# Performance work log

Hardware: AMD Instinct MI355X
Metric: run time of the kernel (lower is better)

Reference implementation:

```python
import jax, jax.numpy as jnp
import numpy as np

S, B, IN, HID, H, D, DFF, L, NC, EMB = 1024, 32, 3072, 256, 16, 16, 1024, 4, 1623, 10


def setup_inputs() -> dict:
    key = jax.random.key(0)
    ks = jax.random.split(key, 12)
    w = lambda k, shp: 0.02 * jax.random.normal(k, shp, dtype=jnp.float32)
    return {
        "x": jax.random.normal(ks[0], (S, B, IN), dtype=jnp.float32),
        "fb": jax.random.randint(ks[1], (S, B), 0, NC),
        "fc1_w": w(ks[2], (HID, IN)),
        "fc1_b": jnp.zeros((HID,), jnp.float32),
        "emb": w(ks[3], (NC, EMB)),
        "proj_w": w(ks[4], (HID, HID + EMB)),
        "proj_b": jnp.zeros((HID,), jnp.float32),
        "ln1_g": jnp.ones((L, HID), jnp.float32),
        "ln1_b": jnp.zeros((L, HID), jnp.float32),
        "slow_w": w(ks[5], (L, H * (3 * D + 1), HID)),
        "out_w": w(ks[6], (L, HID, H * D)),
        "ln2_g": jnp.ones((L, HID), jnp.float32),
        "ln2_b": jnp.zeros((L, HID), jnp.float32),
        "ff1_w": w(ks[7], (L, DFF, HID)),
        "ff1_b": jnp.zeros((L, DFF), jnp.float32),
        "ff2_w": w(ks[8], (L, HID, DFF)),
        "ff2_b": jnp.zeros((L, HID), jnp.float32),
        "outl_w": w(ks[9], (NC, HID)),
        "outl_b": jnp.zeros((NC,), jnp.float32),
    }


def _ln(x, g, b):
    m = jnp.mean(x, -1, keepdims=True)
    v = jnp.mean(jnp.square(x - m), -1, keepdims=True)
    return (x - m) * jax.lax.rsqrt(v + 1e-5) * g + b


def _delta_attn(x, g, b, sw, ow):
    # x: (S, B, HID); delta-rule fast-weight linear attention
    s, bsz, _ = x.shape
    qkvb = jnp.einsum('sbi,oi->sbo', _ln(x, g, b), sw).reshape(s, bsz, H, 3 * D + 1)
    q, k, v, beta = jnp.split(qkvb, [D, 2 * D, 3 * D], axis=-1)
    q = jax.nn.softmax(q, axis=-1)      # sum-normalized feature map
    k = jax.nn.softmax(k, axis=-1)
    beta = jax.nn.sigmoid(beta)         # (S,B,H,1)

    def step(W, inp):
        qt, kt, vt, bt = inp            # (B,H,D),(B,H,D),(B,H,D),(B,H,1)
        v_old = jnp.einsum('bhkv,bhk->bhv', W, kt)
        v_new = bt * vt + (1.0 - bt) * v_old
        W = W + jnp.einsum('bhk,bhv->bhkv', kt, v_new - v_old)
        return W, jnp.einsum('bhkv,bhk->bhv', W, qt)

    W0 = jnp.zeros((bsz, H, D, D), x.dtype)
    _, o = jax.lax.scan(step, W0, (q, k, v, beta))   # o: (S,B,H,D)
    return x + jnp.einsum('sbi,oi->sbo', o.reshape(s, bsz, H * D), ow)


def _ffn(x, g, b, w1, b1, w2, b2):
    h = jax.nn.relu(jnp.einsum('sbi,oi->sbo', _ln(x, g, b), w1) + b1)
    return x + jnp.einsum('sbi,oi->sbo', h, w2) + b2


def reference(x, fb, fc1_w, fc1_b, emb, proj_w, proj_b, ln1_g, ln1_b, slow_w,
              out_w, ln2_g, ln2_b, ff1_w, ff1_b, ff2_w, ff2_b, outl_w, outl_b):
    h = jnp.einsum('sbi,oi->sbo', x, fc1_w) + fc1_b
    h = jnp.concatenate([h, emb[fb]], axis=-1)
    h = jnp.einsum('sbi,oi->sbo', h, proj_w) + proj_b
    for l in range(L):
        h = _delta_attn(h, ln1_g[l], ln1_b[l], slow_w[l], out_w[l])
        h = _ffn(h, ln2_g[l], ln2_b[l], ff1_w[l], ff1_b[l], ff2_w[l], ff2_b[l])
    return jnp.einsum('sbi,oi->sbo', h, outl_w) + outl_b
```

## Files before the change

### kernel.cpp

```cpp
#include <hip/hip_runtime.h>
#include <hip/hip_bf16.h>

#define S_LEN  1024
#define B_SZ   32
#define IN_DIM 3072
#define HID    256
#define NHEAD  16
#define HDIM   16
#define DFF    1024
#define NLAYER 4
#define NCLS   1623
#define EMB_D  10
#define MROWS  (S_LEN * B_SZ)
#define QSTRIDE 52

using bf16   = __hip_bfloat16;
using short8 = __attribute__((ext_vector_type(8))) short;
using f32x4  = __attribute__((ext_vector_type(4))) float;

#define GLOAD16(g, l) __builtin_amdgcn_global_load_lds(                        \
    (const __attribute__((address_space(1))) void*)(g),                        \
    (__attribute__((address_space(3))) void*)(l), 16, 0, 0)

template<int FLAGS>
__global__ __launch_bounds__(256) void mgemm(
    const bf16* __restrict__ A, const bf16* __restrict__ W,
    const float* __restrict__ bias, const float* R, void* C,
    int N, int K, int Wld)
{
    __shared__ bf16 sA[2][128 * 32];
    __shared__ bf16 sB[2][128 * 32];
    const int t    = threadIdx.x;
    const int lane = t & 63;
    const int wid  = t >> 6;
    const int wr   = wid >> 1, wc = wid & 1;
    const long bm  = (long)blockIdx.x * 128;
    const int  bn  = blockIdx.y * 128;
    const int  fr  = lane & 15;
    const int  fg  = lane >> 4;
    const int  row0 = t >> 2;
    const int  kq0  = (t & 3) << 3;

    f32x4 acc[4][4];
#pragma unroll
    for (int m = 0; m < 4; ++m)
#pragma unroll
        for (int n = 0; n < 4; ++n)
#pragma unroll
            for (int r = 0; r < 4; ++r) acc[m][n][r] = 0.f;

    const int nkt = K >> 5;

    auto stage = [&](int buf, int kt) {
        const int k0 = kt << 5;
        GLOAD16(A + (bm + row0)      * (long)K   + k0 + kq0, &sA[buf][(t      ) * 8]);
        GLOAD16(A + (bm + row0 + 64) * (long)K   + k0 + kq0, &sA[buf][(t + 256) * 8]);
        GLOAD16(W + (long)(bn + row0)      * Wld + k0 + kq0, &sB[buf][(t      ) * 8]);
        GLOAD16(W + (long)(bn + row0 + 64) * Wld + k0 + kq0, &sB[buf][(t + 256) * 8]);
    };

    stage(0, 0);
    __syncthreads();
    for (int kt = 0; kt < nkt; ++kt) {
        const int cur = kt & 1;
        if (kt + 1 < nkt) stage(cur ^ 1, kt + 1);
        short8 af[4], bg[4];
#pragma unroll
        for (int m = 0; m < 4; ++m)
            af[m] = *(const short8*)&sA[cur][(wr * 64 + m * 16 + fr) * 32 + fg * 8];
#pragma unroll
        for (int n = 0; n < 4; ++n)
            bg[n] = *(const short8*)&sB[cur][(wc * 64 + n * 16 + fr) * 32 + fg * 8];
#pragma unroll
        for (int m = 0; m < 4; ++m)
#pragma unroll
            for (int n = 0; n < 4; ++n)
                acc[m][n] = __builtin_amdgcn_mfma_f32_16x16x32_bf16(
                    af[m], bg[n], acc[m][n], 0, 0, 0);
        __syncthreads();
    }

    float bs[4];
#pragma unroll
    for (int n = 0; n < 4; ++n) {
        const int c = bn + wc * 64 + n * 16 + fr;
        bs[n] = ((FLAGS & 1) && c < N) ? bias[c] : 0.f;
    }
#pragma unroll
    for (int m = 0; m < 4; ++m) {
#pragma unroll
        for (int n = 0; n < 4; ++n) {
            const int c = bn + wc * 64 + n * 16 + fr;
            if (c < N) {
#pragma unroll
                for (int r = 0; r < 4; ++r) {
                    const long rw = bm + wr * 64 + m * 16 + fg * 4 + r;
                    float v = acc[m][n][r] + bs[n];
                    if (FLAGS & 2) v = fmaxf(v, 0.f);
                    if (FLAGS & 4) v += R[rw * N + c];
                    if (FLAGS & 16) {
                        const int s = (int)(rw >> 5), b = (int)(rw & 31);
                        const int hh = c / 49, cc = c - hh * 49;
                        ((float*)C)[((long)(b * 16 + hh) * 1024 + s) * QSTRIDE + cc] = v;
                    } else if (FLAGS & 8) {
                        ((bf16*)C)[rw * N + c] = __float2bfloat16(v);
                    } else {
                        ((float*)C)[rw * N + c] = v;
                    }
                }
            }
        }
    }
}

__global__ __launch_bounds__(256) void fc1_k(
    const float* __restrict__ A, const bf16* __restrict__ W,
    const float* __restrict__ bias, bf16* __restrict__ C)
{
    __shared__ bf16 sA[2][128 * 32];
    __shared__ bf16 sB[2][128 * 32];
    const int t    = threadIdx.x;
    const int lane = t & 63;
    const int wid  = t >> 6;
    const int wr   = wid >> 1, wc = wid & 1;
    const long bm  = (long)blockIdx.x * 128;
    const int  bn  = blockIdx.y * 128;
    const int  fr  = lane & 15;
    const int  fg  = lane >> 4;
    const int  row0 = t >> 2;
    const int  kq0  = (t & 3) << 3;
    const int  arow = t >> 3;
    const int  ac4  = (t & 7) << 2;

    f32x4 acc[4][4];
#pragma unroll
    for (int m = 0; m < 4; ++m)
#pragma unroll
        for (int n = 0; n < 4; ++n)
#pragma unroll
            for (int r = 0; r < 4; ++r) acc[m][n][r] = 0.f;

    auto stageB = [&](int buf, int kt) {
        const int k0 = kt << 5;
        GLOAD16(W + (long)(bn + row0)      * IN_DIM + k0 + kq0, &sB[buf][(t      ) * 8]);
        GLOAD16(W + (long)(bn + row0 + 64) * IN_DIM + k0 + kq0, &sB[buf][(t + 256) * 8]);
    };
    float4 va[4];
    auto loadA = [&](int kt) {
        const int k0 = kt << 5;
#pragma unroll
        for (int rep = 0; rep < 4; ++rep)
            va[rep] = *(const float4*)(A + (bm + arow + rep * 32) * (long)IN_DIM + k0 + ac4);
    };
    auto writeA = [&](int buf) {
#pragma unroll
        for (int rep = 0; rep < 4; ++rep) {
            alignas(8) bf16 tb[4];
            tb[0] = __float2bfloat16(va[rep].x);
            tb[1] = __float2bfloat16(va[rep].y);
            tb[2] = __float2bfloat16(va[rep].z);
            tb[3] = __float2bfloat16(va[rep].w);
            *(ushort4*)&sA[buf][(arow + rep * 32) * 32 + ac4] = *(const ushort4*)tb;
        }
    };

    loadA(0);
    stageB(0, 0);
    writeA(0);
    __syncthreads();
    const int nkt = IN_DIM >> 5;
    for (int kt = 0; kt < nkt; ++kt) {
        const int cur = kt & 1;
        if (kt + 1 < nkt) { stageB(cur ^ 1, kt + 1); loadA(kt + 1); }
        short8 af[4], bg[4];
#pragma unroll
        for (int m = 0; m < 4; ++m)
            af[m] = *(const short8*)&sA[cur][(wr * 64 + m * 16 + fr) * 32 + fg * 8];
#pragma unroll
        for (int n = 0; n < 4; ++n)
            bg[n] = *(const short8*)&sB[cur][(wc * 64 + n * 16 + fr) * 32 + fg * 8];
#pragma unroll
        for (int m = 0; m < 4; ++m)
#pragma unroll
            for (int n = 0; n < 4; ++n)
                acc[m][n] = __builtin_amdgcn_mfma_f32_16x16x32_bf16(
                    af[m], bg[n], acc[m][n], 0, 0, 0);
        if (kt + 1 < nkt) writeA(cur ^ 1);
        __syncthreads();
    }

#pragma unroll
    for (int n = 0; n < 4; ++n) {
        const int c = bn + wc * 64 + n * 16 + fr;
        const float bsn = bias[c];
#pragma unroll
        for (int m = 0; m < 4; ++m)
#pragma unroll
            for (int r = 0; r < 4; ++r) {
                const long rw = bm + wr * 64 + m * 16 + fg * 4 + r;
                C[rw * HID + c] = __float2bfloat16(acc[m][n][r] + bsn);
            }
    }
}

__global__ __launch_bounds__(256) void cvt8(const float* __restrict__ s,
                                            bf16* __restrict__ d, long n8)
{
    for (long i = (long)blockIdx.x * 256 + threadIdx.x; i < n8;
         i += (long)gridDim.x * 256) {
        const float4 a = ((const float4*)s)[i * 2];
        const float4 b = ((const float4*)s)[i * 2 + 1];
        alignas(16) bf16 t[8];
        t[0] = __float2bfloat16(a.x); t[1] = __float2bfloat16(a.y);
        t[2] = __float2bfloat16(a.z); t[3] = __float2bfloat16(a.w);
        t[4] = __float2bfloat16(b.x); t[5] = __float2bfloat16(b.y);
        t[6] = __float2bfloat16(b.z); t[7] = __float2bfloat16(b.w);
        ((short8*)d)[i] = *(const short8*)t;
    }
}

__global__ __launch_bounds__(256) void cvtpad(const float* __restrict__ s,
                                              bf16* __restrict__ d,
                                              int rows, int cols, int prows, int pcols)
{
    const long tot = (long)prows * pcols;
    for (long i = (long)blockIdx.x * 256 + threadIdx.x; i < tot;
         i += (long)gridDim.x * 256) {
        const int r = (int)(i / pcols), c = (int)(i - (long)r * pcols);
        d[i] = (r < rows && c < cols) ? __float2bfloat16(s[(long)r * cols + c])
                                      : __float2bfloat16(0.f);
    }
}

__global__ __launch_bounds__(256) void cvtpad_slow(const float* __restrict__ s,
                                                   bf16* __restrict__ d)
{
    const int l = blockIdx.y;
    const float* src = s + (size_t)l * 784 * HID;
    bf16* dst = d + (size_t)l * 896 * HID;
    const long tot = (long)896 * HID;
    for (long i = (long)blockIdx.x * 256 + threadIdx.x; i < tot;
         i += (long)gridDim.x * 256) {
        const int r = (int)(i / HID), c = (int)(i - (long)r * HID);
        dst[i] = (r < 784) ? __float2bfloat16(src[(long)r * HID + c])
                           : __float2bfloat16(0.f);
    }
}

__global__ __launch_bounds__(256) void ln_b(
    const float* __restrict__ x, const float* __restrict__ g,
    const float* __restrict__ b, bf16* __restrict__ y)
{
    const int wave = threadIdx.x >> 6, lane = threadIdx.x & 63;
    const long row = (long)(blockIdx.x << 2) + wave;
    const float4 v = ((const float4*)(x + row * HID))[lane];
    float s = v.x + v.y + v.z + v.w;
#pragma unroll
    for (int m = 32; m; m >>= 1) s += __shfl_xor(s, m);
    const float mean = s * (1.f / 256.f);
    const float d0 = v.x - mean, d1 = v.y - mean, d2 = v.z - mean, d3 = v.w - mean;
    float ss = d0 * d0 + d1 * d1 + d2 * d2 + d3 * d3;
#pragma unroll
    for (int m = 32; m; m >>= 1) ss += __shfl_xor(ss, m);
    const float inv = rsqrtf(ss * (1.f / 256.f) + 1e-5f);
    const float4 gg = ((const float4*)g)[lane];
    const float4 bb = ((const float4*)b)[lane];
    alignas(8) bf16 t[4];
    t[0] = __float2bfloat16(fmaf(d0 * inv, gg.x, bb.x));
    t[1] = __float2bfloat16(fmaf(d1 * inv, gg.y, bb.y));
    t[2] = __float2bfloat16(fmaf(d2 * inv, gg.z, bb.z));
    t[3] = __float2bfloat16(fmaf(d3 * inv, gg.w, bb.w));
    *(ushort4*)((unsigned short*)y + row * HID + lane * 4) = *(const ushort4*)t;
}

__global__ __launch_bounds__(64) void concat_b(
    const bf16* __restrict__ ab, const float* __restrict__ emb,
    const int* __restrict__ fb, bf16* __restrict__ hcat)
{
    const long row = blockIdx.x;
    const int lane = threadIdx.x;
    const ushort4 v = ((const ushort4*)(ab + row * HID))[lane];
    ((ushort4*)(hcat + row * 288))[lane] = v;
    if (lane < 32) {
        bf16 val = (lane < EMB_D)
            ? __float2bfloat16(emb[(long)fb[row] * EMB_D + lane])
            : __float2bfloat16(0.f);
        hcat[row * 288 + 256 + lane] = val;
    }
}

#define DOT16(dst, kr, s0, s1, s2, s3) do {                                    \
    float _pa = fmaf(kr[3],  (s0).w, fmaf(kr[2],  (s0).z, fmaf(kr[1],  (s0).y, kr[0]  * (s0).x))); \
    float _pb = fmaf(kr[7],  (s1).w, fmaf(kr[6],  (s1).z, fmaf(kr[5],  (s1).y, kr[4]  * (s1).x))); \
    float _pc = fmaf(kr[11], (s2).w, fmaf(kr[10], (s2).z, fmaf(kr[9],  (s2).y, kr[8]  * (s2).x))); \
    float _pd = fmaf(kr[15], (s3).w, fmaf(kr[14], (s3).z, fmaf(kr[13], (s3).y, kr[12] * (s3).x))); \
    dst = (_pa + _pb) + (_pc + _pd);                                           \
} while (0)

__global__ __launch_bounds__(64) void scan9(
    const float* __restrict__ qkvb, bf16* __restrict__ o)
{
    __shared__ float sbuf[2][1792];
    __shared__ float W0l[16 * 20];
    __shared__ float DVl[16 * 20];
    const int lane = threadIdx.x;
    const int i4 = lane >> 2;
    const int jq = lane & 3;
    const int chain = blockIdx.x;
    const int b = chain >> 4, hh = chain & 15;
    const float* cb = qkvb + (long)chain * S_LEN * QSTRIDE;
    bf16* po = o + (long)b * HID + hh * HDIM + jq * 4;

    for (int z = lane; z < 320; z += 64) W0l[z] = 0.f;

    auto stage = [&](int buf, int nb2) {
#pragma unroll
        for (int iss = 0; iss < 7; ++iss) {
            const float* src = cb + (long)nb2 * 1664 + iss * 256 + lane * 4;
            GLOAD16(src, &sbuf[buf][iss * 256 + lane * 4]);
        }
    };

    stage(0, 0);
    asm volatile("s_waitcnt vmcnt(0)" ::: "memory");
    for (int nb = 0; nb < 32; ++nb) {
        const int buf = nb & 1;
        asm volatile("s_waitcnt vmcnt(2)" ::: "memory");
        if (nb + 1 < 32) stage(buf ^ 1, nb + 1);

        float* sb = sbuf[buf];
        {
            float* p = sb + (lane >> 1) * 52 + ((lane & 1) << 4);
            float4 a0 = *(float4*)(p),     a1 = *(float4*)(p + 4);
            float4 a2 = *(float4*)(p + 8), a3 = *(float4*)(p + 12);
            float mx = fmaxf(fmaxf(fmaxf(a0.x, a0.y), fmaxf(a0.z, a0.w)),
                             fmaxf(fmaxf(a1.x, a1.y), fmaxf(a1.z, a1.w)));
            mx = fmaxf(mx, fmaxf(fmaxf(fmaxf(a2.x, a2.y), fmaxf(a2.z, a2.w)),
                                 fmaxf(fmaxf(a3.x, a3.y), fmaxf(a3.z, a3.w))));
            a0.x = __expf(a0.x - mx); a0.y = __expf(a0.y - mx);
            a0.z = __expf(a0.z - mx); a0.w = __expf(a0.w - mx);
            a1.x = __expf(a1.x - mx); a1.y = __expf(a1.y - mx);
            a1.z = __expf(a1.z - mx); a1.w = __expf(a1.w - mx);
            a2.x = __expf(a2.x - mx); a2.y = __expf(a2.y - mx);
            a2.z = __expf(a2.z - mx); a2.w = __expf(a2.w - mx);
            a3.x = __expf(a3.x - mx); a3.y = __expf(a3.y - mx);
            a3.z = __expf(a3.z - mx); a3.w = __expf(a3.w - mx);
            const float sum = ((a0.x + a0.y) + (a0.z + a0.w))
                            + ((a1.x + a1.y) + (a1.z + a1.w))
                            + ((a2.x + a2.y) + (a2.z + a2.w))
                            + ((a3.x + a3.y) + (a3.z + a3.w));
            const float inv = 1.f / sum;
            a0.x *= inv; a0.y *= inv; a0.z *= inv; a0.w *= inv;
            a1.x *= inv; a1.y *= inv; a1.z *= inv; a1.w *= inv;
            a2.x *= inv; a2.y *= inv; a2.z *= inv; a2.w *= inv;
            a3.x *= inv; a3.y *= inv; a3.z *= inv; a3.w *= inv;
            *(float4*)(p)      = a0; *(float4*)(p + 4)  = a1;
            *(float4*)(p + 8)  = a2; *(float4*)(p + 12) = a3;
            if (!(lane & 1)) p[48] = 1.f / (1.f + __expf(-p[48]));
        }
        asm volatile("s_waitcnt lgkmcnt(0)" ::: "memory");

#pragma unroll
        for (int t = 0; t < 2; ++t) {
            const float* rb = sb + t * 16 * 52;
            const float* myrow = rb + i4 * 52;
            float ki[16], qi[16];
            {
                const float4 kA = *(const float4*)(myrow + 16);
                const float4 kB = *(const float4*)(myrow + 20);
                const float4 kC = *(const float4*)(myrow + 24);
                const float4 kD = *(const float4*)(myrow + 28);
                ki[0]=kA.x; ki[1]=kA.y; ki[2]=kA.z; ki[3]=kA.w;
                ki[4]=kB.x; ki[5]=kB.y; ki[6]=kB.z; ki[7]=kB.w;
                ki[8]=kC.x; ki[9]=kC.y; ki[10]=kC.z; ki[11]=kC.w;
                ki[12]=kD.x; ki[13]=kD.y; ki[14]=kD.z; ki[15]=kD.w;
                const float4 qA = *(const float4*)(myrow);
                const float4 qB = *(const float4*)(myrow + 4);
                const float4 qC = *(const float4*)(myrow + 8);
                const float4 qD = *(const float4*)(myrow + 12);
                qi[0]=qA.x; qi[1]=qA.y; qi[2]=qA.z; qi[3]=qA.w;
                qi[4]=qB.x; qi[5]=qB.y; qi[6]=qB.z; qi[7]=qB.w;
                qi[8]=qC.x; qi[9]=qC.y; qi[10]=qC.z; qi[11]=qC.w;
                qi[12]=qD.x; qi[13]=qD.y; qi[14]=qD.z; qi[15]=qD.w;
            }
            const float beta = myrow[48];
            float gcf[4], qkc[4];
#pragma unroll
            for (int m = 0; m < 4; ++m) {
                const int s = jq * 4 + m;
                const float* sr = rb + s * 52 + 16;
                const float4 s0 = *(const float4*)(sr);
                const float4 s1 = *(const float4*)(sr + 4);
                const float4 s2 = *(const float4*)(sr + 8);
                const float4 s3 = *(const float4*)(sr + 12);
                float g, qk;
                DOT16(g, ki, s0, s1, s2, s3);
                DOT16(qk, qi, s0, s1, s2, s3);
                gcf[m] = (s < i4)  ? -beta * g : 0.f;
                qkc[m] = (s <= i4) ? qk : 0.f;
            }
            float P0=0,P1=0,P2=0,P3=0, O0=0,O1=0,O2=0,O3=0;
#pragma unroll
            for (int x = 0; x < 16; ++x) {
                const float4 w = *(const float4*)&W0l[x * 20 + jq * 4];
                P0 = fmaf(ki[x], w.x, P0); P1 = fmaf(ki[x], w.y, P1);
                P2 = fmaf(ki[x], w.z, P2); P3 = fmaf(ki[x], w.w, P3);
                O0 = fmaf(qi[x], w.x, O0); O1 = fmaf(qi[x], w.y, O1);
                O2 = fmaf(qi[x], w.z, O2); O3 = fmaf(qi[x], w.w, O3);
            }
            const float4 vv = *(const float4*)(myrow + 32 + jq * 4);
            float d0 = beta * (vv.x - P0), d1 = beta * (vv.y - P1);
            float d2 = beta * (vv.z - P2), d3 = beta * (vv.w - P3);
#pragma unroll
            for (int s = 0; s < 15; ++s) {
                const float cf = __shfl(gcf[s & 3], i4 * 4 + (s >> 2));
                const float e0 = __shfl(d0, s * 4 + jq);
                const float e1 = __shfl(d1, s * 4 + jq);
                const float e2 = __shfl(d2, s * 4 + jq);
                const float e3 = __shfl(d3, s * 4 + jq);
                d0 = fmaf(cf, e0, d0); d1 = fmaf(cf, e1, d1);
                d2 = fmaf(cf, e2, d2); d3 = fmaf(cf, e3, d3);
            }
            f32x4 dvv; dvv[0]=d0; dvv[1]=d1; dvv[2]=d2; dvv[3]=d3;
            *(f32x4*)&DVl[i4 * 20 + jq * 4] = dvv;
            asm volatile("s_waitcnt lgkmcnt(0)" ::: "memory");
            float a0=0,a1=0,a2=0,a3=0;
#pragma unroll
            for (int s = 0; s < 16; ++s) {
                const float4 dvs = *(const float4*)&DVl[s * 20 + jq * 4];
                if (s < 15 || true) {
                    const float c = (s == 15)
                        ? ((15 <= i4) ? qkc[3] * 0.f + __shfl(qkc[3], i4 * 4 + 3) * ((i4 == 15) ? 1.f : 0.f) + ((15 < i4) ? 0.f : 0.f) : 0.f)
                        : 0.f;
                    (void)c;
                }
                const float cqk = __shfl(qkc[s & 3], i4 * 4 + (s >> 2));
                O0 = fmaf(cqk, dvs.x, O0); O1 = fmaf(cqk, dvs.y, O1);
                O2 = fmaf(cqk, dvs.z, O2); O3 = fmaf(cqk, dvs.w, O3);
                const float kx = rb[s * 52 + 16 + i4];
                a0 = fmaf(kx, dvs.x, a0); a1 = fmaf(kx, dvs.y, a1);
                a2 = fmaf(kx, dvs.z, a2); a3 = fmaf(kx, dvs.w, a3);
            }
            {
                const int sg = nb * 32 + t * 16 + i4;
                alignas(8) bf16 tb[4];
                tb[0] = __float2bfloat16(O0); tb[1] = __float2bfloat16(O1);
                tb[2] = __float2bfloat16(O2); tb[3] = __float2bfloat16(O3);
                *(ushort4*)((unsigned short*)(po + (long)sg * (B_SZ * HID))) =
                    *(const ushort4*)tb;
            }
            {
                float4 w = *(const float4*)&W0l[i4 * 20 + jq * 4];
                w.x += a0; w.y += a1; w.z += a2; w.w += a3;
                *(float4*)&W0l[i4 * 20 + jq * 4] = w;
            }
            asm volatile("s_waitcnt lgkmcnt(0)" ::: "memory");
        }
    }
}

extern "C" void kernel_launch(void* const* d_in, const int* in_sizes, int n_in,
                              void* d_out, int out_size, void* d_ws, size_t ws_size,
                              hipStream_t stream)
{
    const float* x      = (const float*)d_in[0];
    const int*   fb     = (const int*)  d_in[1];
    const float* fc1_w  = (const float*)d_in[2];
    const float* fc1_b  = (const float*)d_in[3];
    const float* emb    = (const float*)d_in[4];
    const float* proj_w = (const float*)d_in[5];
    const float* proj_b = (const float*)d_in[6];
    const float* ln1_g  = (const float*)d_in[7];
    const float* ln1_b  = (const float*)d_in[8];
    const float* slow_w = (const float*)d_in[9];
    const float* out_w  = (const float*)d_in[10];
    const float* ln2_g  = (const float*)d_in[11];
    const float* ln2_b  = (const float*)d_in[12];
    const float* ff1_w  = (const float*)d_in[13];
    const float* ff1_b  = (const float*)d_in[14];
    const float* ff2_w  = (const float*)d_in[15];
    const float* ff2_b  = (const float*)d_in[16];
    const float* outl_w = (const float*)d_in[17];
    const float* outl_b = (const float*)d_in[18];

    char* wp = (char*)d_ws;
    float* h    = (float*)wp;                 wp += (size_t)MROWS * HID * 4;
    bf16*  abuf = (bf16*)wp;                  wp += (size_t)MROWS * HID * 2;
    bf16*  fc1b = (bf16*)wp;                  wp += (size_t)HID * IN_DIM * 2;
    bf16*  projb= (bf16*)wp;                  wp += (size_t)HID * 288 * 2;
    bf16*  slowb= (bf16*)wp;                  wp += (size_t)NLAYER * 896 * HID * 2;
    bf16*  outwb= (bf16*)wp;                  wp += (size_t)NLAYER * HID * HID * 2;
    bf16*  ff1b = (bf16*)wp;                  wp += (size_t)NLAYER * DFF * HID * 2;
    bf16*  ff2b = (bf16*)wp;                  wp += (size_t)NLAYER * HID * DFF * 2;
    bf16*  outlb= (bf16*)wp;                  wp += (size_t)1664 * HID * 2;

    bf16*  hcat = (bf16*)d_out;
    float* qkvb = (float*)d_out;
    bf16*  hff  = (bf16*)d_out;

    const dim3 blk(256);

    cvt8<<<dim3(384),  blk, 0, stream>>>(fc1_w, fc1b, (long)HID * IN_DIM / 8);
    cvtpad<<<dim3(288), blk, 0, stream>>>(proj_w, projb, HID, HID + EMB_D, HID, 288);
    cvtpad_slow<<<dim3(896, 4), blk, 0, stream>>>(slow_w, slowb);
    cvt8<<<dim3(128), blk, 0, stream>>>(out_w, outwb, (long)NLAYER * HID * HID / 8);
    cvt8<<<dim3(512), blk, 0, stream>>>(ff1_w, ff1b, (long)NLAYER * DFF * HID / 8);
    cvt8<<<dim3(512), blk, 0, stream>>>(ff2_w, ff2b, (long)NLAYER * HID * DFF / 8);
    cvtpad<<<dim3(1664), blk, 0, stream>>>(outl_w, outlb, NCLS, HID, 1664, HID);

    fc1_k<<<dim3(256, 2), blk, 0, stream>>>(x, fc1b, fc1_b, abuf);
    concat_b<<<dim3(MROWS), dim3(64), 0, stream>>>(abuf, emb, fb, hcat);
    mgemm<1><<<dim3(256, 2), blk, 0, stream>>>(hcat, projb, proj_b, nullptr, h,
                                               HID, 288, 288);

    for (int l = 0; l < NLAYER; ++l) {
        ln_b<<<dim3(MROWS / 4), blk, 0, stream>>>(h, ln1_g + l * HID, ln1_b + l * HID, abuf);
        mgemm<16><<<dim3(256, 7), blk, 0, stream>>>(abuf, slowb + (size_t)l * 896 * HID,
                                                    nullptr, nullptr, qkvb, 784, HID, HID);
        scan9<<<dim3(B_SZ * NHEAD), dim3(64), 0, stream>>>(qkvb, abuf);
        mgemm<4><<<dim3(256, 2), blk, 0, stream>>>(abuf, outwb + (size_t)l * HID * HID,
                                                   nullptr, h, h, HID, HID, HID);
        ln_b<<<dim3(MROWS / 4), blk, 0, stream>>>(h, ln2_g + l * HID, ln2_b + l * HID, abuf);
        mgemm<11><<<dim3(256, 8), blk, 0, stream>>>(abuf, ff1b + (size_t)l * DFF * HID,
                                                    ff1_b + l * DFF, nullptr, hff,
                                                    DFF, HID, HID);
        mgemm<5><<<dim3(256, 2), blk, 0, stream>>>(hff, ff2b + (size_t)l * HID * DFF,
                                                   ff2_b + l * HID, h, h, HID, DFF, DFF);
    }
    cvt8<<<dim3(1024), blk, 0, stream>>>(h, abuf, (long)MROWS * HID / 8);
    mgemm<1><<<dim3(256, 13), blk, 0, stream>>>(abuf, outlb, outl_b, nullptr, d_out,
                                                NCLS, HID, HID);
}
```

Before: 1.665 ms.

## Fuse LayerNorm into residual GEMM epilogues and write fc1 directly into concat buffer

```diff
diff --git a/kernel.cpp b/kernel.cpp
--- a/kernel.cpp
+++ b/kernel.cpp
@@ -25,8 +25,7 @@
 template<int FLAGS>
 __global__ __launch_bounds__(256) void mgemm(
     const bf16* __restrict__ A, const bf16* __restrict__ W,
-    const float* __restrict__ bias, const float* R, void* C,
-    int N, int K, int Wld)
+    const float* __restrict__ bias, void* C, int N, int K, int Wld)
 {
     __shared__ bf16 sA[2][128 * 32];
     __shared__ bf16 sB[2][128 * 32];
@@ -97,7 +96,6 @@
                     const long rw = bm + wr * 64 + m * 16 + fg * 4 + r;
                     float v = acc[m][n][r] + bs[n];
                     if (FLAGS & 2) v = fmaxf(v, 0.f);
-                    if (FLAGS & 4) v += R[rw * N + c];
                     if (FLAGS & 16) {
                         const int s = (int)(rw >> 5), b = (int)(rw & 31);
                         const int hh = c / 49, cc = c - hh * 49;
@@ -113,9 +111,148 @@
     }
 }
 
+template<int FLAGS>
+__global__ __launch_bounds__(256) void gemm_ln(
+    const bf16* __restrict__ A, const bf16* __restrict__ W,
+    const float* __restrict__ bias, const float* __restrict__ lg,
+    const float* __restrict__ lb, float* H, bf16* __restrict__ Y, int K)
+{
+    __shared__ bf16 sA[2][64 * 32];
+    __shared__ bf16 sB[2][256 * 32];
+    __shared__ float rsum[64][4];
+    __shared__ float rsq[64][4];
+    const int t    = threadIdx.x;
+    const int lane = t & 63;
+    const int w    = t >> 6;
+    const int fr   = lane & 15;
+    const int fg   = lane >> 4;
+    const long bm  = (long)blockIdx.x * 64;
+
+    f32x4 acc[4][4];
+#pragma unroll
+    for (int m = 0; m < 4; ++m)
+#pragma unroll
+        for (int n = 0; n < 4; ++n)
+#pragma unroll
+            for (int r = 0; r < 4; ++r) acc[m][n][r] = 0.f;
+
+    const int nkt = K >> 5;
+    auto stage = [&](int buf, int kt) {
+        const int k0 = kt << 5;
+        GLOAD16(A + (bm + (t >> 2)) * (long)K + k0 + ((t & 3) << 3),
+                &sA[buf][t * 8]);
+#pragma unroll
+        for (int i = 0; i < 4; ++i)
+            GLOAD16(W + (long)((i << 6) + (t >> 2)) * K + k0 + ((t & 3) << 3),
+                    &sB[buf][(i * 256 + t) * 8]);
+    };
+
+    stage(0, 0);
+    __syncthreads();
+    for (int kt = 0; kt < nkt; ++kt) {
+        const int cur = kt & 1;
+        if (kt + 1 < nkt) stage(cur ^ 1, kt + 1);
+        short8 af[4], bg[4];
+#pragma unroll
+        for (int m = 0; m < 4; ++m)
+            af[m] = *(const short8*)&sA[cur][(m * 16 + fr) * 32 + fg * 8];
+#pragma unroll
+        for (int n = 0; n < 4; ++n)
+            bg[n] = *(const short8*)&sB[cur][(w * 64 + n * 16 + fr) * 32 + fg * 8];
+#pragma unroll
+        for (int m = 0; m < 4; ++m)
+#pragma unroll
+            for (int n = 0; n < 4; ++n)
+                acc[m][n] = __builtin_amdgcn_mfma_f32_16x16x32_bf16(
+                    af[m], bg[n], acc[m][n], 0, 0, 0);
+        __syncthreads();
+    }
+
+    float bs[4];
+#pragma unroll
+    for (int n = 0; n < 4; ++n) {
+        const int c = w * 64 + n * 16 + fr;
+        bs[n] = (FLAGS & 1) ? bias[c] : 0.f;
+    }
+    float ps[4][4], pq[4][4];
+#pragma unroll
+    for (int m = 0; m < 4; ++m)
+#pragma unroll
+        for (int r = 0; r < 4; ++r) { ps[m][r] = 0.f; pq[m][r] = 0.f; }
+#pragma unroll
+    for (int m = 0; m < 4; ++m)
+#pragma unroll
+        for (int n = 0; n < 4; ++n)
+#pragma unroll
+            for (int r = 0; r < 4; ++r) {
+                const long rw = bm + m * 16 + fg * 4 + r;
+                const int c = w * 64 + n * 16 + fr;
+                float v = acc[m][n][r] + bs[n];
+                if (FLAGS & 4) v += H[rw * HID + c];
+                H[rw * HID + c] = v;
+                acc[m][n][r] = v;
+                ps[m][r] += v;
+                pq[m][r] += v * v;
+            }
+    if (FLAGS & 8) {
+#pragma unroll
+        for (int m = 0; m < 4; ++m)
+#pragma unroll
+            for (int n = 0; n < 4; ++n)
+#pragma unroll
+                for (int r = 0; r < 4; ++r) {
+                    const long rw = bm + m * 16 + fg * 4 + r;
+                    const int c = w * 64 + n * 16 + fr;
+                    Y[rw * HID + c] = __float2bfloat16(acc[m][n][r]);
+                }
+    } else {
+#pragma unroll
+        for (int m = 0; m < 4; ++m)
+#pragma unroll
+            for (int r = 0; r < 4; ++r) {
+                float s = ps[m][r], q = pq[m][r];
+                s += __shfl_xor(s, 1); q += __shfl_xor(q, 1);
+                s += __shfl_xor(s, 2); q += __shfl_xor(q, 2);
+                s += __shfl_xor(s, 4); q += __shfl_xor(q, 4);
+                s += __shfl_xor(s, 8); q += __shfl_xor(q, 8);
+                ps[m][r] = s; pq[m][r] = q;
+            }
+        if (fr == 0) {
+#pragma unroll
+            for (int m = 0; m < 4; ++m)
+#pragma unroll
+                for (int r = 0; r < 4; ++r) {
+                    const int row = m * 16 + fg * 4 + r;
+                    rsum[row][w] = ps[m][r];
+                    rsq[row][w]  = pq[m][r];
+                }
+        }
+        __syncthreads();
+#pragma unroll
+        for (int m = 0; m < 4; ++m)
+#pragma unroll
+            for (int r = 0; r < 4; ++r) {
+                const int row = m * 16 + fg * 4 + r;
+                const float4 s4 = *(const float4*)&rsum[row][0];
+                const float4 q4 = *(const float4*)&rsq[row][0];
+                const float S = (s4.x + s4.y) + (s4.z + s4.w);
+                const float Q = (q4.x + q4.y) + (q4.z + q4.w);
+                const float mean = S * (1.f / 256.f);
+                const float inv  = rsqrtf(Q * (1.f / 256.f) - mean * mean + 1e-5f);
+                const long rw = bm + row;
+#pragma unroll
+                for (int n = 0; n < 4; ++n) {
+                    const int c = w * 64 + n * 16 + fr;
+                    const float y = (acc[m][n][r] - mean) * inv * lg[c] + lb[c];
+                    Y[rw * HID + c] = __float2bfloat16(y);
+                }
+            }
+    }
+}
+
 __global__ __launch_bounds__(256) void fc1_k(
     const float* __restrict__ A, const bf16* __restrict__ W,
-    const float* __restrict__ bias, bf16* __restrict__ C)
+    const float* __restrict__ bias, bf16* __restrict__ hcat)
 {
     __shared__ bf16 sA[2][128 * 32];
     __shared__ bf16 sB[2][128 * 32];
@@ -198,9 +335,20 @@
 #pragma unroll
             for (int r = 0; r < 4; ++r) {
                 const long rw = bm + wr * 64 + m * 16 + fg * 4 + r;
-                C[rw * HID + c] = __float2bfloat16(acc[m][n][r] + bsn);
-            }
-    }
+                hcat[rw * 288 + c] = __float2bfloat16(acc[m][n][r] + bsn);
+            }
+    }
+}
+
+__global__ __launch_bounds__(256) void fillemb(
+    const float* __restrict__ emb, const int* __restrict__ fb,
+    bf16* __restrict__ hcat)
+{
+    const long row = (long)blockIdx.x * 8 + (threadIdx.x >> 5);
+    const int c = threadIdx.x & 31;
+    bf16 v = (c < EMB_D) ? __float2bfloat16(emb[(long)fb[row] * EMB_D + c])
+                         : __float2bfloat16(0.f);
+    hcat[row * 288 + 256 + c] = v;
 }
 
 __global__ __launch_bounds__(256) void cvt8(const float* __restrict__ s,
@@ -244,48 +392,6 @@
         const int r = (int)(i / HID), c = (int)(i - (long)r * HID);
         dst[i] = (r < 784) ? __float2bfloat16(src[(long)r * HID + c])
                            : __float2bfloat16(0.f);
-    }
-}
-
-__global__ __launch_bounds__(256) void ln_b(
-    const float* __restrict__ x, const float* __restrict__ g,
-    const float* __restrict__ b, bf16* __restrict__ y)
-{
-    const int wave = threadIdx.x >> 6, lane = threadIdx.x & 63;
-    const long row = (long)(blockIdx.x << 2) + wave;
-    const float4 v = ((const float4*)(x + row * HID))[lane];
-    float s = v.x + v.y + v.z + v.w;
-#pragma unroll
-    for (int m = 32; m; m >>= 1) s += __shfl_xor(s, m);
-    const float mean = s * (1.f / 256.f);
-    const float d0 = v.x - mean, d1 = v.y - mean, d2 = v.z - mean, d3 = v.w - mean;
-    float ss = d0 * d0 + d1 * d1 + d2 * d2 + d3 * d3;
-#pragma unroll
-    for (int m = 32; m; m >>= 1) ss += __shfl_xor(ss, m);
-    const float inv = rsqrtf(ss * (1.f / 256.f) + 1e-5f);
-    const float4 gg = ((const float4*)g)[lane];
-    const float4 bb = ((const float4*)b)[lane];
-    alignas(8) bf16 t[4];
-    t[0] = __float2bfloat16(fmaf(d0 * inv, gg.x, bb.x));
-    t[1] = __float2bfloat16(fmaf(d1 * inv, gg.y, bb.y));
-    t[2] = __float2bfloat16(fmaf(d2 * inv, gg.z, bb.z));
-    t[3] = __float2bfloat16(fmaf(d3 * inv, gg.w, bb.w));
-    *(ushort4*)((unsigned short*)y + row * HID + lane * 4) = *(const ushort4*)t;
-}
-
-__global__ __launch_bounds__(64) void concat_b(
-    const bf16* __restrict__ ab, const float* __restrict__ emb,
-    const int* __restrict__ fb, bf16* __restrict__ hcat)
-{
-    const long row = blockIdx.x;
-    const int lane = threadIdx.x;
-    const ushort4 v = ((const ushort4*)(ab + row * HID))[lane];
-    ((ushort4*)(hcat + row * 288))[lane] = v;
-    if (lane < 32) {
-        bf16 val = (lane < EMB_D)
-            ? __float2bfloat16(emb[(long)fb[row] * EMB_D + lane])
-            : __float2bfloat16(0.f);
-        hcat[row * 288 + 256 + lane] = val;
     }
 }
 
@@ -428,12 +534,6 @@
 #pragma unroll
             for (int s = 0; s < 16; ++s) {
                 const float4 dvs = *(const float4*)&DVl[s * 20 + jq * 4];
-                if (s < 15 || true) {
-                    const float c = (s == 15)
-                        ? ((15 <= i4) ? qkc[3] * 0.f + __shfl(qkc[3], i4 * 4 + 3) * ((i4 == 15) ? 1.f : 0.f) + ((15 < i4) ? 0.f : 0.f) : 0.f)
-                        : 0.f;
-                    (void)c;
-                }
                 const float cqk = __shfl(qkc[s & 3], i4 * 4 + (s >> 2));
                 O0 = fmaf(cqk, dvs.x, O0); O1 = fmaf(cqk, dvs.y, O1);
                 O2 = fmaf(cqk, dvs.z, O2); O3 = fmaf(cqk, dvs.w, O3);
@@ -508,26 +608,30 @@
     cvt8<<<dim3(512), blk, 0, stream>>>(ff2_w, ff2b, (long)NLAYER * HID * DFF / 8);
     cvtpad<<<dim3(1664), blk, 0, stream>>>(outl_w, outlb, NCLS, HID, 1664, HID);
 
-    fc1_k<<<dim3(256, 2), blk, 0, stream>>>(x, fc1b, fc1_b, abuf);
-    concat_b<<<dim3(MROWS), dim3(64), 0, stream>>>(abuf, emb, fb, hcat);
-    mgemm<1><<<dim3(256, 2), blk, 0, stream>>>(hcat, projb, proj_b, nullptr, h,
-                                               HID, 288, 288);
+    fc1_k<<<dim3(256, 2), blk, 0, stream>>>(x, fc1b, fc1_b, hcat);
+    fillemb<<<dim3(MROWS / 8), blk, 0, stream>>>(emb, fb, hcat);
+    gemm_ln<1><<<dim3(512), blk, 0, stream>>>(hcat, projb, proj_b,
+                                              ln1_g, ln1_b, h, abuf, 288);
 
     for (int l = 0; l < NLAYER; ++l) {
-        ln_b<<<dim3(MROWS / 4), blk, 0, stream>>>(h, ln1_g + l * HID, ln1_b + l * HID, abuf);
         mgemm<16><<<dim3(256, 7), blk, 0, stream>>>(abuf, slowb + (size_t)l * 896 * HID,
-                                                    nullptr, nullptr, qkvb, 784, HID, HID);
+                                                    nullptr, qkvb, 784, HID, HID);
         scan9<<<dim3(B_SZ * NHEAD), dim3(64), 0, stream>>>(qkvb, abuf);
-        mgemm<4><<<dim3(256, 2), blk, 0, stream>>>(abuf, outwb + (size_t)l * HID * HID,
-                                                   nullptr, h, h, HID, HID, HID);
-        ln_b<<<dim3(MROWS / 4), blk, 0, stream>>>(h, ln2_g + l * HID, ln2_b + l * HID, abuf);
+        gemm_ln<4><<<dim3(512), blk, 0, stream>>>(abuf, outwb + (size_t)l * HID * HID,
+                                                  nullptr, ln2_g + l * HID,
+                                                  ln2_b + l * HID, h, abuf, HID);
         mgemm<11><<<dim3(256, 8), blk, 0, stream>>>(abuf, ff1b + (size_t)l * DFF * HID,
-                                                    ff1_b + l * DFF, nullptr, hff,
-                                                    DFF, HID, HID);
-        mgemm<5><<<dim3(256, 2), blk, 0, stream>>>(hff, ff2b + (size_t)l * HID * DFF,
-                                                   ff2_b + l * HID, h, h, HID, DFF, DFF);
-    }
-    cvt8<<<dim3(1024), blk, 0, stream>>>(h, abuf, (long)MROWS * HID / 8);
-    mgemm<1><<<dim3(256, 13), blk, 0, stream>>>(abuf, outlb, outl_b, nullptr, d_out,
+                                                    ff1_b + l * DFF, hff, DFF, HID, HID);
+        if (l + 1 < NLAYER)
+            gemm_ln<5><<<dim3(512), blk, 0, stream>>>(hff, ff2b + (size_t)l * HID * DFF,
+                                                      ff2_b + l * HID,
+                                                      ln1_g + (l + 1) * HID,
+                                                      ln1_b + (l + 1) * HID, h, abuf, DFF);
+        else
+            gemm_ln<13><<<dim3(512), blk, 0, stream>>>(hff, ff2b + (size_t)l * HID * DFF,
+                                                       ff2_b + l * HID,
+                                                       nullptr, nullptr, h, abuf, DFF);
+    }
+    mgemm<1><<<dim3(256, 13), blk, 0, stream>>>(abuf, outlb, outl_b, d_out,
                                                 NCLS, HID, HID);
 }
```

New measurement: 1.626 ms. 2.3% less time.
